# Kernel tuning notes

Measured on AMD Instinct MI355X. Metric: run time of the kernel, lower is better.

The kernel has to match this reference:

```python
import jax, jax.numpy as jnp
import numpy as np
import math

D = 512; NA = 128; NC = 256; NB = 128; BATCH = 4; H = 8
EA, EC, EB = 4, 6, 4
KA, KC, KB = 2, 1, 2
F = 4 * D  # expert_ff_mult * embed_dim
N_TOTAL = NA + NC + NB


def setup_inputs() -> dict:
    key = jax.random.key(0)
    ks = jax.random.split(key, 16)
    s = 0.02
    def nrm(k, shape, scale=s):
        return jax.random.normal(k, shape, dtype=jnp.float32) * scale
    return {
        'tokens_A': jax.random.normal(ks[0], (BATCH, NA, D), dtype=jnp.float32),
        'tokens_B': jax.random.normal(ks[1], (BATCH, NB, D), dtype=jnp.float32),
        'tokens_C': jax.random.normal(ks[2], (BATCH, NC, D), dtype=jnp.float32),
        'ln1_g': jnp.ones((3, D), jnp.float32), 'ln1_b': jnp.zeros((3, D), jnp.float32),
        'ln2_g': jnp.ones((3, D), jnp.float32), 'ln2_b': jnp.zeros((3, D), jnp.float32),
        'Wqkv': nrm(ks[3], (3 * D, D)), 'bqkv': jnp.zeros((3 * D,), jnp.float32),
        'Wo': nrm(ks[4], (D, D)), 'bo': jnp.zeros((D,), jnp.float32),
        'Wr_A': nrm(ks[5], (D, EA)), 'br_A': jnp.zeros((EA,), jnp.float32),
        'W1_A': nrm(ks[6], (EA, D, F)), 'b1_A': jnp.zeros((EA, F), jnp.float32),
        'W2_A': nrm(ks[7], (EA, F, D)), 'b2_A': jnp.zeros((EA, D), jnp.float32),
        'Wr_C': nrm(ks[8], (D, EC)), 'br_C': jnp.zeros((EC,), jnp.float32),
        'W1_C': nrm(ks[9], (EC, D, F)), 'b1_C': jnp.zeros((EC, F), jnp.float32),
        'W2_C': nrm(ks[10], (EC, F, D)), 'b2_C': jnp.zeros((EC, D), jnp.float32),
        'Wr_B': nrm(ks[11], (D, EB)), 'br_B': jnp.zeros((EB,), jnp.float32),
        'W1_B': nrm(ks[12], (EB, D, F)), 'b1_B': jnp.zeros((EB, F), jnp.float32),
        'W2_B': nrm(ks[13], (EB, F, D)), 'b2_B': jnp.zeros((EB, D), jnp.float32),
    }


def _ln(x, g, b, eps=1e-5):
    m = jnp.mean(x, axis=-1, keepdims=True)
    v = jnp.var(x, axis=-1, keepdims=True)
    return (x - m) * jax.lax.rsqrt(v + eps) * g + b


def _directed_mask_bias():
    # segments: 0=A, 1=C, 2=B in [A|C|B] order; query may attend upstream groups only
    seg = jnp.concatenate([jnp.zeros(NA), jnp.ones(NC), 2.0 * jnp.ones(NB)])
    allowed = seg[None, :] <= seg[:, None]  # (N, N)
    return jnp.where(allowed, 0.0, -1e9).astype(jnp.float32)


def _mha(x, Wqkv, bqkv, Wo, bo, mask_bias):
    B, N, _ = x.shape
    qkv = x @ Wqkv.T + bqkv  # (B, N, 3D)
    q, k, v = jnp.split(qkv, 3, axis=-1)
    hd = D // H
    def heads(t):
        return t.reshape(B, N, H, hd).transpose(0, 2, 1, 3)  # (B, H, N, hd)
    q, k, v = heads(q), heads(k), heads(v)
    scores = jnp.einsum('bhqd,bhkd->bhqk', q, k) / math.sqrt(hd) + mask_bias[None, None]
    attn = jax.nn.softmax(scores, axis=-1)
    o = jnp.einsum('bhqk,bhkd->bhqd', attn, v).transpose(0, 2, 1, 3).reshape(B, N, D)
    return o @ Wo.T + bo


def _moe(x, Wr, br, W1, b1, W2, b2, k):
    # top-k routed expert FFN: softmax gates -> top-k renormalized -> dense combine
    probs = jax.nn.softmax(x @ Wr + br, axis=-1)  # (B, N, E)
    vals, idx = jax.lax.top_k(probs, k)
    vals = vals / jnp.sum(vals, axis=-1, keepdims=True)
    E = Wr.shape[1]
    gate = jnp.sum(jax.nn.one_hot(idx, E, dtype=x.dtype) * vals[..., None], axis=-2)  # (B, N, E)
    h = jax.nn.gelu(jnp.einsum('bnd,edf->benf', x, W1) + b1[None, :, None, :])
    y = jnp.einsum('benf,efd->bend', h, W2) + b2[None, :, None, :]
    return jnp.einsum('bne,bend->bnd', gate, y)


def reference(tokens_A, tokens_B, tokens_C, ln1_g, ln1_b, ln2_g, ln2_b,
              Wqkv, bqkv, Wo, bo,
              Wr_A, br_A, W1_A, b1_A, W2_A, b2_A,
              Wr_C, br_C, W1_C, b1_C, W2_C, b2_C,
              Wr_B, br_B, W1_B, b1_B, W2_B, b2_B):
    # 1-2. group-local pre-attention LN, concat [A | C | B]
    x = jnp.concatenate([
        _ln(tokens_A, ln1_g[0], ln1_b[0]),
        _ln(tokens_C, ln1_g[1], ln1_b[1]),
        _ln(tokens_B, ln1_g[2], ln1_b[2]),
    ], axis=1)
    # 3-4. shared directed self-attention + per-group residual
    attn = _mha(x, Wqkv, bqkv, Wo, bo, _directed_mask_bias())
    tA = tokens_A + attn[:, :NA]
    tC = tokens_C + attn[:, NA:NA + NC]
    tB = tokens_B + attn[:, NA + NC:]
    # 5. group-local pre-expert LN
    nA = _ln(tA, ln2_g[0], ln2_b[0])
    nC = _ln(tC, ln2_g[1], ln2_b[1])
    nB = _ln(tB, ln2_g[2], ln2_b[2])
    # 6-9. route A and C first, then B; residual add per group
    tA = tA + _moe(nA, Wr_A, br_A, W1_A, b1_A, W2_A, b2_A, KA)
    tC = tC + _moe(nC, Wr_C, br_C, W1_C, b1_C, W2_C, b2_C, KC)
    tB = tB + _moe(nB, Wr_B, br_B, W1_B, b1_B, W2_B, b2_B, KB)
    return jnp.concatenate([tA, tC, tB], axis=1)  # (B, NA+NC+NB, D)
```

## Files before the change

kernel.cpp:

```cpp
#include <hip/hip_runtime.h>
#include <hip/hip_bf16.h>
#include <cstdint>

#define DEV __device__ __forceinline__

using f32x4  = __attribute__((ext_vector_type(4))) float;
using bf16x8 = __attribute__((ext_vector_type(8))) __bf16;

static constexpr int D_    = 512;
static constexpr int ROWS  = 2048;
static constexpr int F_    = 2048;
static constexpr int NEXP  = 14;
static constexpr int NENT  = 3072;

DEV unsigned short f2bf(float f) {
  unsigned int u = __builtin_bit_cast(unsigned int, f);
  unsigned int r = u + 0x7FFFu + ((u >> 16) & 1u);
  return (unsigned short)(r >> 16);
}
DEV unsigned int pack2(float a, float b) {
  return (unsigned int)f2bf(a) | ((unsigned int)f2bf(b) << 16);
}
DEV float gelu_tanh(float x) {
  float x3 = x * x * x;
  return 0.5f * x * (1.0f + tanhf(0.7978845608028654f * (x + 0.044715f * x3)));
}

struct Shared128 { unsigned short As[128][72]; unsigned short Bs[64][72]; };

DEV void gemm128(const unsigned short* arow, const float* B, int ldb, int bcol0, int K,
                 f32x4 (&acc)[2][4], Shared128& sh)
{
  const int tid = threadIdx.x;
  const int lane = tid & 63, w = tid >> 6;
  const int ai = tid >> 1, ah = tid & 1;
  const int bj = tid >> 2, bq = tid & 3;
  for (int k0 = 0; k0 < K; k0 += 64) {
    __syncthreads();
    {
      const uint4* src = reinterpret_cast<const uint4*>(arow + k0 + ah * 32);
      uint4 v0 = src[0], v1 = src[1], v2 = src[2], v3 = src[3];
      uint4* dst = reinterpret_cast<uint4*>(&sh.As[ai][ah * 32]);
      dst[0] = v0; dst[1] = v1; dst[2] = v2; dst[3] = v3;
    }
    {
      const float4* src = reinterpret_cast<const float4*>(B + (size_t)(bcol0 + bj) * ldb + k0 + bq * 16);
      unsigned int pk[8];
      #pragma unroll
      for (int u = 0; u < 4; ++u) {
        float4 f = src[u];
        pk[u * 2]     = pack2(f.x, f.y);
        pk[u * 2 + 1] = pack2(f.z, f.w);
      }
      uint4* dst = reinterpret_cast<uint4*>(&sh.Bs[bj][bq * 16]);
      dst[0] = make_uint4(pk[0], pk[1], pk[2], pk[3]);
      dst[1] = make_uint4(pk[4], pk[5], pk[6], pk[7]);
    }
    __syncthreads();
    #pragma unroll
    for (int ks = 0; ks < 2; ++ks) {
      bf16x8 a[2], b[4];
      #pragma unroll
      for (int mi = 0; mi < 2; ++mi)
        a[mi] = *reinterpret_cast<const bf16x8*>(&sh.As[w * 32 + mi * 16 + (lane & 15)][ks * 32 + (lane >> 4) * 8]);
      #pragma unroll
      for (int ni = 0; ni < 4; ++ni)
        b[ni] = *reinterpret_cast<const bf16x8*>(&sh.Bs[ni * 16 + (lane & 15)][ks * 32 + (lane >> 4) * 8]);
      #pragma unroll
      for (int mi = 0; mi < 2; ++mi)
        #pragma unroll
        for (int ni = 0; ni < 4; ++ni)
          acc[mi][ni] = __builtin_amdgcn_mfma_f32_16x16x32_bf16(a[mi], b[ni], acc[mi][ni], 0, 0, 0);
    }
  }
}

struct Shared64 { unsigned short As[64][72]; unsigned short Bs[64][72]; };

DEV void gemm64(const unsigned short* arow, const unsigned short* B, int ldb, int bcol0, int K,
                f32x4 (&acc)[4], Shared64& sh)
{
  const int tid = threadIdx.x;
  const int lane = tid & 63, w = tid >> 6;
  const int rr = tid >> 2, qq = tid & 3;
  for (int k0 = 0; k0 < K; k0 += 64) {
    __syncthreads();
    {
      const uint4* srcA = reinterpret_cast<const uint4*>(arow + k0 + qq * 16);
      uint4 a0 = srcA[0], a1 = srcA[1];
      uint4* dstA = reinterpret_cast<uint4*>(&sh.As[rr][qq * 16]);
      dstA[0] = a0; dstA[1] = a1;
      const uint4* srcB = reinterpret_cast<const uint4*>(B + (size_t)(bcol0 + rr) * ldb + k0 + qq * 16);
      uint4 b0 = srcB[0], b1 = srcB[1];
      uint4* dstB = reinterpret_cast<uint4*>(&sh.Bs[rr][qq * 16]);
      dstB[0] = b0; dstB[1] = b1;
    }
    __syncthreads();
    #pragma unroll
    for (int ks = 0; ks < 2; ++ks) {
      bf16x8 a = *reinterpret_cast<const bf16x8*>(&sh.As[w * 16 + (lane & 15)][ks * 32 + (lane >> 4) * 8]);
      #pragma unroll
      for (int ni = 0; ni < 4; ++ni) {
        bf16x8 b = *reinterpret_cast<const bf16x8*>(&sh.Bs[ni * 16 + (lane & 15)][ks * 32 + (lane >> 4) * 8]);
        acc[ni] = __builtin_amdgcn_mfma_f32_16x16x32_bf16(a, b, acc[ni], 0, 0, 0);
      }
    }
  }
}

__global__ __launch_bounds__(256) void k_ln(
    const float* tA, const float* tC, const float* tB, const float* tfull,
    const float* g3, const float* b3, unsigned short* out, int mode)
{
  int r = blockIdx.x;
  int b = r >> 9, n = r & 511;
  int grp = n < 128 ? 0 : (n < 384 ? 1 : 2);
  const float* src;
  if (mode == 0) {
    src = grp == 0 ? tA + (size_t)(b * 128 + n) * D_
        : grp == 1 ? tC + (size_t)(b * 256 + n - 128) * D_
                   : tB + (size_t)(b * 128 + n - 384) * D_;
  } else {
    src = tfull + (size_t)r * D_;
  }
  int tid = threadIdx.x, lane = tid & 63, w = tid >> 6;
  float2 v = *reinterpret_cast<const float2*>(src + tid * 2);
  float s = v.x + v.y;
  float ss = v.x * v.x + v.y * v.y;
  #pragma unroll
  for (int off = 1; off < 64; off <<= 1) { s += __shfl_xor(s, off); ss += __shfl_xor(ss, off); }
  __shared__ float red[8];
  if (lane == 0) { red[w] = s; red[4 + w] = ss; }
  __syncthreads();
  float S  = red[0] + red[1] + red[2] + red[3];
  float SS = red[4] + red[5] + red[6] + red[7];
  float mean = S * (1.0f / 512.0f);
  float var  = SS * (1.0f / 512.0f) - mean * mean;
  float inv  = rsqrtf(var + 1e-5f);
  const float* gam = g3 + grp * D_;
  const float* bet = b3 + grp * D_;
  int d0 = tid * 2;
  out[(size_t)r * D_ + d0]     = f2bf((v.x - mean) * inv * gam[d0]     + bet[d0]);
  out[(size_t)r * D_ + d0 + 1] = f2bf((v.y - mean) * inv * gam[d0 + 1] + bet[d0 + 1]);
}

__global__ __launch_bounds__(256) void k_qkv(const unsigned short* x, const float* Wqkv, const float* bqkv,
                                             unsigned short* Qg, unsigned short* Kg, unsigned short* Vg)
{
  __shared__ Shared128 sh;
  int bn = blockIdx.x, bm = blockIdx.y, batch = blockIdx.z;
  int tid = threadIdx.x, lane = tid & 63, w = tid >> 6;
  const unsigned short* arow = x + (size_t)(batch * 512 + bm * 128 + (tid >> 1)) * D_;
  f32x4 acc[2][4] = {};
  gemm128(arow, Wqkv, 512, bn * 64, 512, acc, sh);
  #pragma unroll
  for (int mi = 0; mi < 2; ++mi)
  #pragma unroll
  for (int ni = 0; ni < 4; ++ni)
  #pragma unroll
  for (int j = 0; j < 4; ++j) {
    int n = bm * 128 + w * 32 + mi * 16 + ((lane >> 4) << 2) + j;
    int col = bn * 64 + ni * 16 + (lane & 15);
    float val = acc[mi][ni][j] + bqkv[col];
    int part = col >> 9;
    int o = col & 511, h = o >> 6, d = o & 63;
    unsigned short* dst = part == 0 ? Qg : (part == 1 ? Kg : Vg);
    dst[(size_t)((batch * 8 + h) * 512 + n) * 64 + d] = f2bf(val);
  }
}

__global__ __launch_bounds__(256) void k_attn(const unsigned short* Qg, const unsigned short* Kg,
                                              const unsigned short* Vg, unsigned short* attn)
{
  __shared__ unsigned short Qs[64][72], Ks[64][72], VT[64][72], Ps[64][72];
  int qt = blockIdx.x, h = blockIdx.y, b = blockIdx.z;
  int tid = threadIdx.x, lane = tid & 63, w = tid >> 6;
  const unsigned short* Qb  = Qg + (size_t)((b * 8 + h) * 512) * 64;
  const unsigned short* Kbp = Kg + (size_t)((b * 8 + h) * 512) * 64;
  const unsigned short* Vbp = Vg + (size_t)((b * 8 + h) * 512) * 64;
  int i4 = tid >> 2, q4 = tid & 3;
  {
    const uint4* src = reinterpret_cast<const uint4*>(Qb + (size_t)(qt * 64 + i4) * 64 + q4 * 16);
    uint4 v0 = src[0], v1 = src[1];
    uint4* dst = reinterpret_cast<uint4*>(&Qs[i4][q4 * 16]);
    dst[0] = v0; dst[1] = v1;
  }
  int nkt = qt < 2 ? 2 : (qt < 6 ? 6 : 8);
  float mrun[4] = { -1e30f, -1e30f, -1e30f, -1e30f };
  float lrun[4] = {};
  f32x4 o[4] = {};
  for (int kt = 0; kt < nkt; ++kt) {
    __syncthreads();
    {
      const uint4* src = reinterpret_cast<const uint4*>(Kbp + (size_t)(kt * 64 + i4) * 64 + q4 * 16);
      uint4 v0 = src[0], v1 = src[1];
      uint4* dst = reinterpret_cast<uint4*>(&Ks[i4][q4 * 16]);
      dst[0] = v0; dst[1] = v1;
      union { uint4 u[2]; unsigned short s[16]; } vv;
      const uint4* vsrc = reinterpret_cast<const uint4*>(Vbp + (size_t)(kt * 64 + i4) * 64 + q4 * 16);
      vv.u[0] = vsrc[0]; vv.u[1] = vsrc[1];
      #pragma unroll
      for (int jj = 0; jj < 16; ++jj) VT[q4 * 16 + jj][i4] = vv.s[jj];
    }
    __syncthreads();
    f32x4 s[4] = {};
    #pragma unroll
    for (int ks = 0; ks < 2; ++ks) {
      bf16x8 aq = *reinterpret_cast<const bf16x8*>(&Qs[w * 16 + (lane & 15)][ks * 32 + (lane >> 4) * 8]);
      #pragma unroll
      for (int cc = 0; cc < 4; ++cc) {
        bf16x8 bk = *reinterpret_cast<const bf16x8*>(&Ks[cc * 16 + (lane & 15)][ks * 32 + (lane >> 4) * 8]);
        s[cc] = __builtin_amdgcn_mfma_f32_16x16x32_bf16(aq, bk, s[cc], 0, 0, 0);
      }
    }
    #pragma unroll
    for (int rr = 0; rr < 4; ++rr) {
      float s0 = s[0][rr] * 0.125f, s1 = s[1][rr] * 0.125f;
      float s2 = s[2][rr] * 0.125f, s3 = s[3][rr] * 0.125f;
      float mx = fmaxf(fmaxf(s0, s1), fmaxf(s2, s3));
      #pragma unroll
      for (int off = 1; off < 16; off <<= 1) mx = fmaxf(mx, __shfl_xor(mx, off));
      float mn = fmaxf(mrun[rr], mx);
      float al = expf(mrun[rr] - mn);
      mrun[rr] = mn;
      float p0 = expf(s0 - mn), p1 = expf(s1 - mn), p2 = expf(s2 - mn), p3 = expf(s3 - mn);
      float ps = p0 + p1 + p2 + p3;
      #pragma unroll
      for (int off = 1; off < 16; off <<= 1) ps += __shfl_xor(ps, off);
      lrun[rr] = lrun[rr] * al + ps;
      #pragma unroll
      for (int n4 = 0; n4 < 4; ++n4) o[n4][rr] *= al;
      int prow = w * 16 + ((lane >> 4) << 2) + rr;
      Ps[prow][0 * 16 + (lane & 15)] = f2bf(p0);
      Ps[prow][1 * 16 + (lane & 15)] = f2bf(p1);
      Ps[prow][2 * 16 + (lane & 15)] = f2bf(p2);
      Ps[prow][3 * 16 + (lane & 15)] = f2bf(p3);
    }
    __syncthreads();
    #pragma unroll
    for (int ks = 0; ks < 2; ++ks) {
      bf16x8 ap = *reinterpret_cast<const bf16x8*>(&Ps[w * 16 + (lane & 15)][ks * 32 + (lane >> 4) * 8]);
      #pragma unroll
      for (int n4 = 0; n4 < 4; ++n4) {
        bf16x8 bv = *reinterpret_cast<const bf16x8*>(&VT[n4 * 16 + (lane & 15)][ks * 32 + (lane >> 4) * 8]);
        o[n4] = __builtin_amdgcn_mfma_f32_16x16x32_bf16(ap, bv, o[n4], 0, 0, 0);
      }
    }
  }
  #pragma unroll
  for (int n4 = 0; n4 < 4; ++n4)
  #pragma unroll
  for (int rr = 0; rr < 4; ++rr) {
    int qrow = qt * 64 + w * 16 + ((lane >> 4) << 2) + rr;
    int col = h * 64 + n4 * 16 + (lane & 15);
    float val = o[n4][rr] / lrun[rr];
    attn[(size_t)(b * 512 + qrow) * 512 + col] = f2bf(val);
  }
}

__global__ __launch_bounds__(256) void k_wo(const unsigned short* attn, const float* Wo, const float* bo,
                                            const float* tokA, const float* tokC, const float* tokB,
                                            float* out)
{
  __shared__ Shared128 sh;
  int bn = blockIdx.x, bm = blockIdx.y;
  int tid = threadIdx.x, lane = tid & 63, w = tid >> 6;
  const unsigned short* arow = attn + (size_t)(bm * 128 + (tid >> 1)) * D_;
  f32x4 acc[2][4] = {};
  gemm128(arow, Wo, 512, bn * 64, 512, acc, sh);
  #pragma unroll
  for (int mi = 0; mi < 2; ++mi)
  #pragma unroll
  for (int ni = 0; ni < 4; ++ni)
  #pragma unroll
  for (int j = 0; j < 4; ++j) {
    int row = bm * 128 + w * 32 + mi * 16 + ((lane >> 4) << 2) + j;
    int col = bn * 64 + ni * 16 + (lane & 15);
    float val = acc[mi][ni][j] + bo[col];
    int b = row >> 9, n = row & 511;
    float res;
    if (n < 128)      res = tokA[(size_t)(b * 128 + n) * D_ + col];
    else if (n < 384) res = tokC[(size_t)(b * 256 + n - 128) * D_ + col];
    else              res = tokB[(size_t)(b * 128 + n - 384) * D_ + col];
    out[(size_t)row * D_ + col] = res + val;
  }
}

template<int E, int TOPK, int EGBASE, int SEG0, int NSEG>
__global__ __launch_bounds__(256) void k_router(const float* t,
    const float* ln2g, const float* ln2b, const float* Wr, const float* br,
    int* cnt, int* tokexp, float* tokgate)
{
  constexpr int GRP = EGBASE == 0 ? 0 : (EGBASE == 4 ? 1 : 2);
  constexpr int BPB = NSEG / 4;
  int w = threadIdx.x >> 6, lane = threadIdx.x & 63;
  int b = blockIdx.x / BPB, i = blockIdx.x % BPB;
  int r = b * 512 + SEG0 + i * 4 + w;
  const float* tr = t + (size_t)r * D_;
  float xv[8];
  float s = 0.0f, ss = 0.0f;
  #pragma unroll
  for (int it = 0; it < 8; ++it) {
    float v = tr[it * 64 + lane];
    xv[it] = v; s += v; ss += v * v;
  }
  #pragma unroll
  for (int off = 1; off < 64; off <<= 1) { s += __shfl_xor(s, off); ss += __shfl_xor(ss, off); }
  float mean = s * (1.0f / 512.0f);
  float var  = ss * (1.0f / 512.0f) - mean * mean;
  float inv  = rsqrtf(var + 1e-5f);
  const float* gam = ln2g + GRP * D_;
  const float* bet = ln2b + GRP * D_;
  float acc[E] = {};
  #pragma unroll
  for (int it = 0; it < 8; ++it) {
    int d = it * 64 + lane;
    float nv = (xv[it] - mean) * inv * gam[d] + bet[d];
    #pragma unroll
    for (int e = 0; e < E; ++e) acc[e] += nv * Wr[d * E + e];
  }
  #pragma unroll
  for (int e = 0; e < E; ++e)
    #pragma unroll
    for (int off = 1; off < 64; off <<= 1) acc[e] += __shfl_xor(acc[e], off);
  if (lane == 0) {
    float p[E];
    float mx = -1e30f;
    #pragma unroll
    for (int e = 0; e < E; ++e) { p[e] = acc[e] + br[e]; mx = fmaxf(mx, p[e]); }
    float sum = 0.0f;
    #pragma unroll
    for (int e = 0; e < E; ++e) { p[e] = expf(p[e] - mx); sum += p[e]; }
    #pragma unroll
    for (int e = 0; e < E; ++e) p[e] /= sum;
    int i1 = 0; float v1 = p[0];
    #pragma unroll
    for (int e = 1; e < E; ++e) if (p[e] > v1) { v1 = p[e]; i1 = e; }
    if (TOPK == 1) {
      tokexp[r * 2]     = EGBASE + i1; tokgate[r * 2]     = 1.0f;
      tokexp[r * 2 + 1] = -1;          tokgate[r * 2 + 1] = 0.0f;
      atomicAdd(&cnt[EGBASE + i1], 1);
    } else {
      int i2 = -1; float v2 = -1e30f;
      #pragma unroll
      for (int e = 0; e < E; ++e) if (e != i1 && p[e] > v2) { v2 = p[e]; i2 = e; }
      float tot = v1 + v2;
      tokexp[r * 2]     = EGBASE + i1; tokgate[r * 2]     = v1 / tot;
      tokexp[r * 2 + 1] = EGBASE + i2; tokgate[r * 2 + 1] = v2 / tot;
      atomicAdd(&cnt[EGBASE + i1], 1);
      atomicAdd(&cnt[EGBASE + i2], 1);
    }
  }
}

__global__ void k_scan(const int* cnt, int* base) {
  if (threadIdx.x == 0) {
    int acc = 0;
    for (int e = 0; e < NEXP; ++e) { base[e] = acc; acc += cnt[e]; }
  }
}
__global__ __launch_bounds__(256) void k_scatter(const int* tokexp, const float* tokgate,
                                                 const int* base, int* cursor, int* list, float* gate)
{
  int r = blockIdx.x * 256 + threadIdx.x;
  #pragma unroll
  for (int j = 0; j < 2; ++j) {
    int e = tokexp[r * 2 + j];
    if (e >= 0) {
      int s = atomicAdd(&cursor[e], 1);
      list[base[e] + s] = r;
      gate[base[e] + s] = tokgate[r * 2 + j];
    }
  }
}

__global__ __launch_bounds__(256) void k_trAll(
    const float* w1A, const float* w1C, const float* w1B,
    const float* w2A, const float* w2C, const float* w2B,
    unsigned short* W1T, unsigned short* W2T)
{
  int bx = blockIdx.x, by = blockIdx.y, z = blockIdx.z;
  const float* src;
  unsigned short* dst;
  int ldS, ldD, R0, C0;
  if (z < 14) {
    int e = z;
    src = e < 4 ? w1A + (size_t)e * D_ * F_ : e < 10 ? w1C + (size_t)(e - 4) * D_ * F_ : w1B + (size_t)(e - 10) * D_ * F_;
    dst = W1T + (size_t)e * F_ * D_;
    ldS = F_; ldD = D_;
    R0 = by * 64;
    C0 = bx * 64;
  } else {
    int e = z - 14;
    src = e < 4 ? w2A + (size_t)e * F_ * D_ : e < 10 ? w2C + (size_t)(e - 4) * F_ * D_ : w2B + (size_t)(e - 10) * F_ * D_;
    dst = W2T + (size_t)e * D_ * F_;
    ldS = D_; ldD = F_;
    R0 = bx * 64;
    C0 = by * 64;
  }
  __shared__ float tile[64][65];
  int t = threadIdx.x, r = t >> 2, q = t & 3;
  const float4* sp = reinterpret_cast<const float4*>(src + (size_t)(R0 + r) * ldS + C0 + q * 16);
  #pragma unroll
  for (int u = 0; u < 4; ++u) {
    float4 v = sp[u];
    tile[r][q * 16 + u * 4 + 0] = v.x; tile[r][q * 16 + u * 4 + 1] = v.y;
    tile[r][q * 16 + u * 4 + 2] = v.z; tile[r][q * 16 + u * 4 + 3] = v.w;
  }
  __syncthreads();
  int c = t >> 2;
  unsigned int pk[8];
  #pragma unroll
  for (int i = 0; i < 8; ++i) {
    float fa = tile[q * 16 + 2 * i][c];
    float fb = tile[q * 16 + 2 * i + 1][c];
    pk[i] = pack2(fa, fb);
  }
  uint4* dp = reinterpret_cast<uint4*>(dst + (size_t)(C0 + c) * ldD + R0 + q * 16);
  dp[0] = make_uint4(pk[0], pk[1], pk[2], pk[3]);
  dp[1] = make_uint4(pk[4], pk[5], pk[6], pk[7]);
}

__global__ __launch_bounds__(256) void k_moe1(const unsigned short* nrm, const unsigned short* W1T,
    const float* b1A, const float* b1C, const float* b1B,
    const int* cnt, const int* ebase, const int* list, unsigned short* H)
{
  int ft = blockIdx.x, tt = blockIdx.y, e = blockIdx.z;
  int c = cnt[e];
  if (tt * 64 >= c) return;
  __shared__ Shared64 sh;
  const float* b1 = e < 4 ? b1A + (size_t)e * F_ : e < 10 ? b1C + (size_t)(e - 4) * F_ : b1B + (size_t)(e - 10) * F_;
  const unsigned short* Wt = W1T + (size_t)e * F_ * D_;
  int base = ebase[e];
  int tid = threadIdx.x, lane = tid & 63, w = tid >> 6;
  int ig = tt * 64 + (tid >> 2);
  int tok = list[base + (ig < c ? ig : c - 1)];
  const unsigned short* arow = nrm + (size_t)tok * D_;
  f32x4 acc[4] = {};
  gemm64(arow, Wt, 512, ft * 64, 512, acc, sh);
  #pragma unroll
  for (int ni = 0; ni < 4; ++ni)
  #pragma unroll
  for (int j = 0; j < 4; ++j) {
    int rl = w * 16 + ((lane >> 4) << 2) + j;
    int sg = tt * 64 + rl;
    if (sg < c) {
      int col = ft * 64 + ni * 16 + (lane & 15);
      float val = acc[ni][j] + b1[col];
      H[(size_t)(base + sg) * F_ + col] = f2bf(gelu_tanh(val));
    }
  }
}

__global__ __launch_bounds__(256) void k_moe2(const unsigned short* H, const unsigned short* W2T,
    const float* b2A, const float* b2C, const float* b2B,
    const int* cnt, const int* ebase, const int* list, const float* gate, float* out)
{
  int dt = blockIdx.x, tt = blockIdx.y >> 2, kc = blockIdx.y & 3, e = blockIdx.z;
  int c = cnt[e];
  if (tt * 64 >= c) return;
  __shared__ Shared64 sh;
  const float* b2 = e < 4 ? b2A + (size_t)e * D_ : e < 10 ? b2C + (size_t)(e - 4) * D_ : b2B + (size_t)(e - 10) * D_;
  const unsigned short* Wt = W2T + (size_t)e * D_ * F_ + kc * 512;
  int base = ebase[e];
  int tid = threadIdx.x, lane = tid & 63, w = tid >> 6;
  int ig = tt * 64 + (tid >> 2);
  const unsigned short* arow = H + (size_t)(base + (ig < c ? ig : c - 1)) * F_ + kc * 512;
  f32x4 acc[4] = {};
  gemm64(arow, Wt, F_, dt * 64, 512, acc, sh);
  #pragma unroll
  for (int ni = 0; ni < 4; ++ni)
  #pragma unroll
  for (int j = 0; j < 4; ++j) {
    int rl = w * 16 + ((lane >> 4) << 2) + j;
    int sg = tt * 64 + rl;
    if (sg < c) {
      int col = dt * 64 + ni * 16 + (lane & 15);
      float val = acc[ni][j] + (kc == 0 ? b2[col] : 0.0f);
      int tok = list[base + sg];
      atomicAdd(&out[(size_t)tok * D_ + col], gate[base + sg] * val);
    }
  }
}

extern "C" void kernel_launch(void* const* d_in, const int* in_sizes, int n_in,
                              void* d_out, int out_size, void* d_ws, size_t ws_size,
                              hipStream_t stream)
{
  const float* tokA = (const float*)d_in[0];
  const float* tokB = (const float*)d_in[1];
  const float* tokC = (const float*)d_in[2];
  const float* ln1g = (const float*)d_in[3];
  const float* ln1b = (const float*)d_in[4];
  const float* ln2g = (const float*)d_in[5];
  const float* ln2b = (const float*)d_in[6];
  const float* Wqkv = (const float*)d_in[7];
  const float* bqkv = (const float*)d_in[8];
  const float* Wo   = (const float*)d_in[9];
  const float* bo   = (const float*)d_in[10];
  const float* WrA  = (const float*)d_in[11];
  const float* brA  = (const float*)d_in[12];
  const float* W1A  = (const float*)d_in[13];
  const float* b1A  = (const float*)d_in[14];
  const float* W2A  = (const float*)d_in[15];
  const float* b2A  = (const float*)d_in[16];
  const float* WrC  = (const float*)d_in[17];
  const float* brC  = (const float*)d_in[18];
  const float* W1C  = (const float*)d_in[19];
  const float* b1C  = (const float*)d_in[20];
  const float* W2C  = (const float*)d_in[21];
  const float* b2C  = (const float*)d_in[22];
  const float* WrB  = (const float*)d_in[23];
  const float* brB  = (const float*)d_in[24];
  const float* W1B  = (const float*)d_in[25];
  const float* b1B  = (const float*)d_in[26];
  const float* W2B  = (const float*)d_in[27];
  const float* b2B  = (const float*)d_in[28];
  float* out = (float*)d_out;

  char* ws = (char*)d_ws;
  const size_t MB = 1024 * 1024;
  const size_t WSTRIDE = (size_t)NEXP * F_ * D_ * 2;
  unsigned short* xb   = (unsigned short*)(ws);
  unsigned short* nrm  = xb;
  unsigned short* Qg   = (unsigned short*)(ws + 2 * MB);
  unsigned short* Kg   = (unsigned short*)(ws + 4 * MB);
  unsigned short* Vg   = (unsigned short*)(ws + 6 * MB);
  unsigned short* attn = (unsigned short*)(ws + 8 * MB);
  unsigned short* W1T  = (unsigned short*)(ws + 16 * MB);
  unsigned short* W2T  = (unsigned short*)(ws + 16 * MB + WSTRIDE);
  unsigned short* H    = (unsigned short*)(ws + 16 * MB + 2 * WSTRIDE);
  char* small = ws + 16 * MB + 2 * WSTRIDE + (size_t)NENT * F_ * 2;
  int*   cnt     = (int*)(small);
  int*   cursor  = (int*)(small + 64);
  int*   ebase   = (int*)(small + 128);
  int*   tokexp  = (int*)(small + 256);
  float* tokgate = (float*)(small + 256 + ROWS * 2 * 4);
  int*   list    = (int*)(small + 256 + ROWS * 4 * 4);
  float* gate    = (float*)(small + 256 + ROWS * 4 * 4 + NENT * 4);

  hipMemsetAsync(cnt, 0, 192, stream);
  k_ln<<<ROWS, 256, 0, stream>>>(tokA, tokC, tokB, nullptr, ln1g, ln1b, xb, 0);
  k_qkv<<<dim3(24, 4, 4), 256, 0, stream>>>(xb, Wqkv, bqkv, Qg, Kg, Vg);
  k_attn<<<dim3(8, 8, 4), 256, 0, stream>>>(Qg, Kg, Vg, attn);
  k_wo<<<dim3(8, 16), 256, 0, stream>>>(attn, Wo, bo, tokA, tokC, tokB, out);
  k_ln<<<ROWS, 256, 0, stream>>>(nullptr, nullptr, nullptr, out, ln2g, ln2b, nrm, 1);
  k_router<4, 2, 0,  0,   128><<<128, 256, 0, stream>>>(out, ln2g, ln2b, WrA, brA, cnt, tokexp, tokgate);
  k_router<6, 1, 4,  128, 256><<<256, 256, 0, stream>>>(out, ln2g, ln2b, WrC, brC, cnt, tokexp, tokgate);
  k_router<4, 2, 10, 384, 128><<<128, 256, 0, stream>>>(out, ln2g, ln2b, WrB, brB, cnt, tokexp, tokgate);
  k_scan<<<1, 64, 0, stream>>>(cnt, ebase);
  k_scatter<<<8, 256, 0, stream>>>(tokexp, tokgate, ebase, cursor, list, gate);
  k_trAll<<<dim3(32, 8, 28), 256, 0, stream>>>(W1A, W1C, W1B, W2A, W2C, W2B, W1T, W2T);
  k_moe1<<<dim3(32, 16, 14), 256, 0, stream>>>(nrm, W1T, b1A, b1C, b1B, cnt, ebase, list, H);
  k_moe2<<<dim3(8, 64, 14), 256, 0, stream>>>(H, W2T, b2A, b2C, b2B, cnt, ebase, list, gate, out);
}
```

Before: 230.8 us.

## Widen MoE GEMM tiles to 64x128, fuse LN2 into router, retile weight transpose

The MoE expert GEMMs now use 64x128 output tiles, so each block reuses its A tile across twice as many columns and the grid is halved. The second layernorm kernel is removed, and the router kernels now write the normalized bf16 activations they already compute, saving a launch and a full read of the residual stream. The weight transpose kernel is retiled to 128x32 tiles with a flattened grid. Larger tiles raise register use and shrink the block count, which can reduce occupancy.

```diff
diff --git a/kernel.cpp b/kernel.cpp
--- a/kernel.cpp
+++ b/kernel.cpp
@@ -75,32 +75,33 @@
   }
 }
 
-struct Shared64 { unsigned short As[64][72]; unsigned short Bs[64][72]; };
-
-DEV void gemm64(const unsigned short* arow, const unsigned short* B, int ldb, int bcol0, int K,
-                f32x4 (&acc)[4], Shared64& sh)
+struct Shared64x128 { unsigned short As[64][72]; unsigned short Bs[128][72]; };
+
+DEV void gemm64x128(const unsigned short* arow, const unsigned short* B, int ldb, int bcol0, int K,
+                    f32x4 (&acc)[8], Shared64x128& sh)
 {
   const int tid = threadIdx.x;
   const int lane = tid & 63, w = tid >> 6;
-  const int rr = tid >> 2, qq = tid & 3;
+  const int ar = tid >> 2, aq = tid & 3;
+  const int br = tid >> 1, bh = tid & 1;
   for (int k0 = 0; k0 < K; k0 += 64) {
     __syncthreads();
     {
-      const uint4* srcA = reinterpret_cast<const uint4*>(arow + k0 + qq * 16);
+      const uint4* srcA = reinterpret_cast<const uint4*>(arow + k0 + aq * 16);
       uint4 a0 = srcA[0], a1 = srcA[1];
-      uint4* dstA = reinterpret_cast<uint4*>(&sh.As[rr][qq * 16]);
+      uint4* dstA = reinterpret_cast<uint4*>(&sh.As[ar][aq * 16]);
       dstA[0] = a0; dstA[1] = a1;
-      const uint4* srcB = reinterpret_cast<const uint4*>(B + (size_t)(bcol0 + rr) * ldb + k0 + qq * 16);
-      uint4 b0 = srcB[0], b1 = srcB[1];
-      uint4* dstB = reinterpret_cast<uint4*>(&sh.Bs[rr][qq * 16]);
-      dstB[0] = b0; dstB[1] = b1;
+      const uint4* srcB = reinterpret_cast<const uint4*>(B + (size_t)(bcol0 + br) * ldb + k0 + bh * 32);
+      uint4 b0 = srcB[0], b1 = srcB[1], b2 = srcB[2], b3 = srcB[3];
+      uint4* dstB = reinterpret_cast<uint4*>(&sh.Bs[br][bh * 32]);
+      dstB[0] = b0; dstB[1] = b1; dstB[2] = b2; dstB[3] = b3;
     }
     __syncthreads();
     #pragma unroll
     for (int ks = 0; ks < 2; ++ks) {
       bf16x8 a = *reinterpret_cast<const bf16x8*>(&sh.As[w * 16 + (lane & 15)][ks * 32 + (lane >> 4) * 8]);
       #pragma unroll
-      for (int ni = 0; ni < 4; ++ni) {
+      for (int ni = 0; ni < 8; ++ni) {
         bf16x8 b = *reinterpret_cast<const bf16x8*>(&sh.Bs[ni * 16 + (lane & 15)][ks * 32 + (lane >> 4) * 8]);
         acc[ni] = __builtin_amdgcn_mfma_f32_16x16x32_bf16(a, b, acc[ni], 0, 0, 0);
       }
@@ -109,20 +110,15 @@
 }
 
 __global__ __launch_bounds__(256) void k_ln(
-    const float* tA, const float* tC, const float* tB, const float* tfull,
-    const float* g3, const float* b3, unsigned short* out, int mode)
+    const float* tA, const float* tC, const float* tB,
+    const float* g3, const float* b3, unsigned short* out)
 {
   int r = blockIdx.x;
   int b = r >> 9, n = r & 511;
   int grp = n < 128 ? 0 : (n < 384 ? 1 : 2);
-  const float* src;
-  if (mode == 0) {
-    src = grp == 0 ? tA + (size_t)(b * 128 + n) * D_
-        : grp == 1 ? tC + (size_t)(b * 256 + n - 128) * D_
-                   : tB + (size_t)(b * 128 + n - 384) * D_;
-  } else {
-    src = tfull + (size_t)r * D_;
-  }
+  const float* src = grp == 0 ? tA + (size_t)(b * 128 + n) * D_
+                   : grp == 1 ? tC + (size_t)(b * 256 + n - 128) * D_
+                              : tB + (size_t)(b * 128 + n - 384) * D_;
   int tid = threadIdx.x, lane = tid & 63, w = tid >> 6;
   float2 v = *reinterpret_cast<const float2*>(src + tid * 2);
   float s = v.x + v.y;
@@ -289,7 +285,7 @@
 template<int E, int TOPK, int EGBASE, int SEG0, int NSEG>
 __global__ __launch_bounds__(256) void k_router(const float* t,
     const float* ln2g, const float* ln2b, const float* Wr, const float* br,
-    int* cnt, int* tokexp, float* tokgate)
+    int* cnt, int* tokexp, float* tokgate, unsigned short* nrm)
 {
   constexpr int GRP = EGBASE == 0 ? 0 : (EGBASE == 4 ? 1 : 2);
   constexpr int BPB = NSEG / 4;
@@ -316,6 +312,7 @@
   for (int it = 0; it < 8; ++it) {
     int d = it * 64 + lane;
     float nv = (xv[it] - mean) * inv * gam[d] + bet[d];
+    nrm[(size_t)r * D_ + d] = f2bf(nv);
     #pragma unroll
     for (int e = 0; e < E; ++e) acc[e] += nv * Wr[d * E + e];
   }
@@ -379,7 +376,7 @@
     const float* w2A, const float* w2C, const float* w2B,
     unsigned short* W1T, unsigned short* W2T)
 {
-  int bx = blockIdx.x, by = blockIdx.y, z = blockIdx.z;
+  int bx = blockIdx.x, z = blockIdx.y;
   const float* src;
   unsigned short* dst;
   int ldS, ldD, R0, C0;
@@ -388,37 +385,42 @@
     src = e < 4 ? w1A + (size_t)e * D_ * F_ : e < 10 ? w1C + (size_t)(e - 4) * D_ * F_ : w1B + (size_t)(e - 10) * D_ * F_;
     dst = W1T + (size_t)e * F_ * D_;
     ldS = F_; ldD = D_;
-    R0 = by * 64;
-    C0 = bx * 64;
+    R0 = (bx & 3) * 128;
+    C0 = (bx >> 2) * 32;
   } else {
     int e = z - 14;
     src = e < 4 ? w2A + (size_t)e * F_ * D_ : e < 10 ? w2C + (size_t)(e - 4) * F_ * D_ : w2B + (size_t)(e - 10) * F_ * D_;
     dst = W2T + (size_t)e * D_ * F_;
     ldS = D_; ldD = F_;
-    R0 = bx * 64;
-    C0 = by * 64;
-  }
-  __shared__ float tile[64][65];
-  int t = threadIdx.x, r = t >> 2, q = t & 3;
-  const float4* sp = reinterpret_cast<const float4*>(src + (size_t)(R0 + r) * ldS + C0 + q * 16);
-  #pragma unroll
-  for (int u = 0; u < 4; ++u) {
-    float4 v = sp[u];
-    tile[r][q * 16 + u * 4 + 0] = v.x; tile[r][q * 16 + u * 4 + 1] = v.y;
-    tile[r][q * 16 + u * 4 + 2] = v.z; tile[r][q * 16 + u * 4 + 3] = v.w;
+    R0 = (bx & 15) * 128;
+    C0 = (bx >> 4) * 32;
+  }
+  __shared__ float tile[128][33];
+  int t = threadIdx.x;
+  {
+    int r = t >> 1, h = t & 1;
+    const float4* sp = reinterpret_cast<const float4*>(src + (size_t)(R0 + r) * ldS + C0 + h * 16);
+    #pragma unroll
+    for (int u = 0; u < 4; ++u) {
+      float4 v = sp[u];
+      tile[r][h * 16 + u * 4 + 0] = v.x; tile[r][h * 16 + u * 4 + 1] = v.y;
+      tile[r][h * 16 + u * 4 + 2] = v.z; tile[r][h * 16 + u * 4 + 3] = v.w;
+    }
   }
   __syncthreads();
-  int c = t >> 2;
-  unsigned int pk[8];
-  #pragma unroll
-  for (int i = 0; i < 8; ++i) {
-    float fa = tile[q * 16 + 2 * i][c];
-    float fb = tile[q * 16 + 2 * i + 1][c];
-    pk[i] = pack2(fa, fb);
-  }
-  uint4* dp = reinterpret_cast<uint4*>(dst + (size_t)(C0 + c) * ldD + R0 + q * 16);
-  dp[0] = make_uint4(pk[0], pk[1], pk[2], pk[3]);
-  dp[1] = make_uint4(pk[4], pk[5], pk[6], pk[7]);
+  {
+    int c = t >> 3, g = t & 7;
+    unsigned int pk[8];
+    #pragma unroll
+    for (int i = 0; i < 8; ++i) {
+      float fa = tile[g * 16 + 2 * i][c];
+      float fb = tile[g * 16 + 2 * i + 1][c];
+      pk[i] = pack2(fa, fb);
+    }
+    uint4* dp = reinterpret_cast<uint4*>(dst + (size_t)(C0 + c) * ldD + R0 + g * 16);
+    dp[0] = make_uint4(pk[0], pk[1], pk[2], pk[3]);
+    dp[1] = make_uint4(pk[4], pk[5], pk[6], pk[7]);
+  }
 }
 
 __global__ __launch_bounds__(256) void k_moe1(const unsigned short* nrm, const unsigned short* W1T,
@@ -428,7 +430,7 @@
   int ft = blockIdx.x, tt = blockIdx.y, e = blockIdx.z;
   int c = cnt[e];
   if (tt * 64 >= c) return;
-  __shared__ Shared64 sh;
+  __shared__ Shared64x128 sh;
   const float* b1 = e < 4 ? b1A + (size_t)e * F_ : e < 10 ? b1C + (size_t)(e - 4) * F_ : b1B + (size_t)(e - 10) * F_;
   const unsigned short* Wt = W1T + (size_t)e * F_ * D_;
   int base = ebase[e];
@@ -436,16 +438,16 @@
   int ig = tt * 64 + (tid >> 2);
   int tok = list[base + (ig < c ? ig : c - 1)];
   const unsigned short* arow = nrm + (size_t)tok * D_;
-  f32x4 acc[4] = {};
-  gemm64(arow, Wt, 512, ft * 64, 512, acc, sh);
-  #pragma unroll
-  for (int ni = 0; ni < 4; ++ni)
+  f32x4 acc[8] = {};
+  gemm64x128(arow, Wt, 512, ft * 128, 512, acc, sh);
+  #pragma unroll
+  for (int ni = 0; ni < 8; ++ni)
   #pragma unroll
   for (int j = 0; j < 4; ++j) {
     int rl = w * 16 + ((lane >> 4) << 2) + j;
     int sg = tt * 64 + rl;
     if (sg < c) {
-      int col = ft * 64 + ni * 16 + (lane & 15);
+      int col = ft * 128 + ni * 16 + (lane & 15);
       float val = acc[ni][j] + b1[col];
       H[(size_t)(base + sg) * F_ + col] = f2bf(gelu_tanh(val));
     }
@@ -459,23 +461,23 @@
   int dt = blockIdx.x, tt = blockIdx.y >> 2, kc = blockIdx.y & 3, e = blockIdx.z;
   int c = cnt[e];
   if (tt * 64 >= c) return;
-  __shared__ Shared64 sh;
+  __shared__ Shared64x128 sh;
   const float* b2 = e < 4 ? b2A + (size_t)e * D_ : e < 10 ? b2C + (size_t)(e - 4) * D_ : b2B + (size_t)(e - 10) * D_;
   const unsigned short* Wt = W2T + (size_t)e * D_ * F_ + kc * 512;
   int base = ebase[e];
   int tid = threadIdx.x, lane = tid & 63, w = tid >> 6;
   int ig = tt * 64 + (tid >> 2);
   const unsigned short* arow = H + (size_t)(base + (ig < c ? ig : c - 1)) * F_ + kc * 512;
-  f32x4 acc[4] = {};
-  gemm64(arow, Wt, F_, dt * 64, 512, acc, sh);
-  #pragma unroll
-  for (int ni = 0; ni < 4; ++ni)
+  f32x4 acc[8] = {};
+  gemm64x128(arow, Wt, F_, dt * 128, 512, acc, sh);
+  #pragma unroll
+  for (int ni = 0; ni < 8; ++ni)
   #pragma unroll
   for (int j = 0; j < 4; ++j) {
     int rl = w * 16 + ((lane >> 4) << 2) + j;
     int sg = tt * 64 + rl;
     if (sg < c) {
-      int col = dt * 64 + ni * 16 + (lane & 15);
+      int col = dt * 128 + ni * 16 + (lane & 15);
       float val = acc[ni][j] + (kc == 0 ? b2[col] : 0.0f);
       int tok = list[base + sg];
       atomicAdd(&out[(size_t)tok * D_ + col], gate[base + sg] * val);
@@ -540,17 +542,16 @@
   float* gate    = (float*)(small + 256 + ROWS * 4 * 4 + NENT * 4);
 
   hipMemsetAsync(cnt, 0, 192, stream);
-  k_ln<<<ROWS, 256, 0, stream>>>(tokA, tokC, tokB, nullptr, ln1g, ln1b, xb, 0);
+  k_ln<<<ROWS, 256, 0, stream>>>(tokA, tokC, tokB, ln1g, ln1b, xb);
   k_qkv<<<dim3(24, 4, 4), 256, 0, stream>>>(xb, Wqkv, bqkv, Qg, Kg, Vg);
   k_attn<<<dim3(8, 8, 4), 256, 0, stream>>>(Qg, Kg, Vg, attn);
   k_wo<<<dim3(8, 16), 256, 0, stream>>>(attn, Wo, bo, tokA, tokC, tokB, out);
-  k_ln<<<ROWS, 256, 0, stream>>>(nullptr, nullptr, nullptr, out, ln2g, ln2b, nrm, 1);
-  k_router<4, 2, 0,  0,   128><<<128, 256, 0, stream>>>(out, ln2g, ln2b, WrA, brA, cnt, tokexp, tokgate);
-  k_router<6, 1, 4,  128, 256><<<256, 256, 0, stream>>>(out, ln2g, ln2b, WrC, brC, cnt, tokexp, tokgate);
-  k_router<4, 2, 10, 384, 128><<<128, 256, 0, stream>>>(out, ln2g, ln2b, WrB, brB, cnt, tokexp, tokgate);
+  k_router<4, 2, 0,  0,   128><<<128, 256, 0, stream>>>(out, ln2g, ln2b, WrA, brA, cnt, tokexp, tokgate, nrm);
+  k_router<6, 1, 4,  128, 256><<<256, 256, 0, stream>>>(out, ln2g, ln2b, WrC, brC, cnt, tokexp, tokgate, nrm);
+  k_router<4, 2, 10, 384, 128><<<128, 256, 0, stream>>>(out, ln2g, ln2b, WrB, brB, cnt, tokexp, tokgate, nrm);
   k_scan<<<1, 64, 0, stream>>>(cnt, ebase);
   k_scatter<<<8, 256, 0, stream>>>(tokexp, tokgate, ebase, cursor, list, gate);
-  k_trAll<<<dim3(32, 8, 28), 256, 0, stream>>>(W1A, W1C, W1B, W2A, W2C, W2B, W1T, W2T);
-  k_moe1<<<dim3(32, 16, 14), 256, 0, stream>>>(nrm, W1T, b1A, b1C, b1B, cnt, ebase, list, H);
-  k_moe2<<<dim3(8, 64, 14), 256, 0, stream>>>(H, W2T, b2A, b2C, b2B, cnt, ebase, list, gate, out);
-}
+  k_trAll<<<dim3(256, 28), 256, 0, stream>>>(W1A, W1C, W1B, W2A, W2C, W2B, W1T, W2T);
+  k_moe1<<<dim3(16, 16, 14), 256, 0, stream>>>(nrm, W1T, b1A, b1C, b1B, cnt, ebase, list, H);
+  k_moe2<<<dim3(4, 64, 14), 256, 0, stream>>>(H, W2T, b2A, b2C, b2B, cnt, ebase, list, gate, out);
+}
```

After: 236.9 us. +2.6%, slower.
